# Optimization experiments

Measured on AMD Instinct MI355X. Metric: run time of the kernel, lower is better.

## Reference

```python
import jax, jax.numpy as jnp
import numpy as np

NUM_EXPERTS = 64
Z_LOSS_COEF = 0.001
AUX_LOSS_COEF = 0.001
GROUPS, TOKENS = 64, 8192


def setup_inputs() -> dict:
    key = jax.random.key(0)
    k1, = jax.random.split(key, 1)
    router_logits = jax.random.normal(k1, (GROUPS, TOKENS, NUM_EXPERTS), dtype=jnp.float32)
    attention_mask = jnp.ones((GROUPS, TOKENS), dtype=jnp.int32)  # unused by forward, kept for fidelity
    return {"router_logits": router_logits, "attention_mask": attention_mask, "expert_capacity": 160}


def reference(router_logits, attention_mask, expert_capacity):
    g, t, e = router_logits.shape

    # --- router z-loss: mean over (groups, tokens) of logsumexp^2 ---
    log_z = jax.nn.logsumexp(router_logits, axis=-1)            # [g, t]
    z_loss = jnp.sum(log_z * log_z) / (g * t)

    # --- softmax probs ---
    router_probs = jax.nn.softmax(router_logits, axis=-1)       # [g, t, e]

    # --- recompute expert indices with capacity masking ---
    expert_index = jnp.argmax(router_probs, axis=-1)            # [g, t]
    oh = jax.nn.one_hot(expert_index, e, dtype=jnp.int32)       # [g, t, e]
    token_priority = jnp.cumsum(oh, axis=-2)                    # running count per expert
    capacity_mask = token_priority <= expert_capacity
    oh_masked = oh * capacity_mask.astype(jnp.int32)
    # if token dropped (row all zero), argmax -> 0, matching torch semantics
    expert_index = jnp.argmax(oh_masked, axis=-1)               # [g, t]

    # --- load-balancing aux loss ---
    expert_mask = jax.nn.one_hot(expert_index, e, dtype=jnp.float32)  # [g, t, e]
    tokens_per_group_and_expert = jnp.mean(expert_mask, axis=-2)       # [g, e]
    router_prob_per_group_and_expert = jnp.mean(router_probs, axis=-2) # [g, e]
    aux_loss = jnp.mean(tokens_per_group_and_expert * router_prob_per_group_and_expert) * (e ** 2)

    return Z_LOSS_COEF * z_loss + AUX_LOSS_COEF * aux_loss
```

## Files before the change

kernel.cpp:

```cpp
#include <hip/hip_runtime.h>

#define NG 64
#define NT 8192
#define NE 64
#define Z_COEF 0.001f
#define A_COEF 0.001f

#define BLK 512
#define ITERS 4
#define TPW 64
#define TPB 512
#define NBLK (NG * (NT / TPB))

#define LOG2E 1.44269504088896340736f
#define LN2   0.69314718055994530942f
#define BIGIDX 1048576

#define DPP_XOR1  0xB1
#define DPP_XOR2  0x4E
#define DPP_HMIRR 0x141
#define DPP_MIRR  0x140

template <int CTRL>
__device__ __forceinline__ float fdpp(float x) {
    return __int_as_float(__builtin_amdgcn_mov_dpp(__float_as_int(x), CTRL, 0xF, 0xF, true));
}
template <int CTRL>
__device__ __forceinline__ int idpp(int x) {
    return __builtin_amdgcn_mov_dpp(x, CTRL, 0xF, 0xF, true);
}


__global__ __launch_bounds__(BLK) void router_main(
    const float* __restrict__ logits,
    float* __restrict__ pps,
    unsigned int* __restrict__ pcnt,
    float* __restrict__ pz,
    float* __restrict__ accbuf,
    unsigned int* __restrict__ donep)
{
    const int tid  = threadIdx.x;
    const int lane = tid & 63;
    const int wv   = tid >> 6;
    const int c    = lane & 15;
    const int cb   = c << 2;

    if (blockIdx.x == 0 && tid == 0) {
        accbuf[0] = 0.f;
        accbuf[1] = 0.f;
        *donep    = 0u;
    }

    const int g     = blockIdx.x >> 4;
    const int tbase = (blockIdx.x & 15) * TPB + wv * TPW;

    const float* p0 = logits + ((size_t)g * NT + tbase) * NE + lane * 4;

    __shared__ float        s_ps[NE];
    __shared__ unsigned int s_cnt[NE];
    __shared__ float        s_z;
    if (tid < NE) { s_ps[tid] = 0.f; s_cnt[tid] = 0u; }
    if (tid == 0) s_z = 0.f;
    __syncthreads();

    float accp[4] = {0.f, 0.f, 0.f, 0.f};
    float accz = 0.f;

    for (int it = 0; it < ITERS; ++it) {
        const float* pi = p0 + (size_t)it * 1024;
        float4 cur[4];
#pragma unroll
        for (int k = 0; k < 4; ++k)
            cur[k] = *reinterpret_cast<const float4*>(pi + k * 256);

#pragma unroll
        for (int k = 0; k < 4; ++k) {
            const float v0 = cur[k].x, v1 = cur[k].y, v2 = cur[k].z, v3 = cur[k].w;

            float m = fmaxf(fmaxf(v0, v1), fmaxf(v2, v3));
            m = fmaxf(m, fdpp<DPP_XOR1>(m));
            m = fmaxf(m, fdpp<DPP_XOR2>(m));
            m = fmaxf(m, fdpp<DPP_HMIRR>(m));
            m = fmaxf(m, fdpp<DPP_MIRR>(m));

            const float e0 = exp2f((v0 - m) * LOG2E);
            const float e1 = exp2f((v1 - m) * LOG2E);
            const float e2 = exp2f((v2 - m) * LOG2E);
            const float e3 = exp2f((v3 - m) * LOG2E);
            float s = (e0 + e1) + (e2 + e3);

            int me = BIGIDX;
            if (v3 == m) me = cb + 3;
            if (v2 == m) me = cb + 2;
            if (v1 == m) me = cb + 1;
            if (v0 == m) me = cb + 0;
            me = min(me, idpp<DPP_XOR1>(me));
            me = min(me, idpp<DPP_XOR2>(me));
            me = min(me, idpp<DPP_HMIRR>(me));
            me = min(me, idpp<DPP_MIRR>(me));

            s += fdpp<DPP_XOR1>(s);
            s += fdpp<DPP_XOR2>(s);
            s += fdpp<DPP_HMIRR>(s);
            s += fdpp<DPP_MIRR>(s);

            const float inv = __builtin_amdgcn_rcpf(s);
            accp[0] = fmaf(e0, inv, accp[0]);
            accp[1] = fmaf(e1, inv, accp[1]);
            accp[2] = fmaf(e2, inv, accp[2]);
            accp[3] = fmaf(e3, inv, accp[3]);

            const float lz = fmaf(__log2f(s), LN2, m);
            accz = fmaf(lz, lz, accz);

            if (c == 0)
                atomicAdd(&s_cnt[me], 1u);
        }
    }

#pragma unroll
    for (int j = 0; j < 4; ++j) {
        accp[j] += __shfl_xor(accp[j], 16);
        accp[j] += __shfl_xor(accp[j], 32);
    }
    if (lane < 16) {
#pragma unroll
        for (int j = 0; j < 4; ++j) atomicAdd(&s_ps[cb + j], accp[j]);
    }
    accz += __shfl_xor(accz, 1);
    accz += __shfl_xor(accz, 2);
    accz += __shfl_xor(accz, 4);
    accz += __shfl_xor(accz, 8);
    accz += __shfl_xor(accz, 16);
    accz += __shfl_xor(accz, 32);
    if (lane == 0) atomicAdd(&s_z, accz * 0.0625f);
    __syncthreads();

    const int row = blockIdx.x;
    if (tid < NE) {
        pps [row * NE + tid] = s_ps[tid];
        pcnt[row * NE + tid] = s_cnt[tid];
    }
    if (tid == 0) pz[row] = s_z;
}

__global__ __launch_bounds__(64) void router_final(
    const float* __restrict__ pps,
    const unsigned int* __restrict__ pcnt,
    const float* __restrict__ pz,
    const int* __restrict__ capp,
    float* __restrict__ accbuf,
    unsigned int* __restrict__ donep,
    float* __restrict__ out)
{
    const int lane = threadIdx.x;
    const int g    = blockIdx.x;
    const unsigned int C = (unsigned int)(*capp);

    unsigned int n = 0u;
    float        P = 0.f;
#pragma unroll
    for (int b = 0; b < 16; ++b) {
        const int row = g * 16 + b;
        n += pcnt[row * NE + lane];
        P += pps [row * NE + lane];
    }

    float ovf = (n > C) ? (float)(n - C) : 0.f;
#pragma unroll
    for (int off = 1; off <= 32; off <<= 1) ovf += __shfl_xor(ovf, off);

    float ce = fminf((float)n, (float)C);
    if (lane == 0) ce += ovf;
    float term = ce * P;
#pragma unroll
    for (int off = 1; off <= 32; off <<= 1) term += __shfl_xor(term, off);

    float zz = (lane < 16) ? pz[g * 16 + lane] : 0.f;
#pragma unroll
    for (int off = 1; off <= 8; off <<= 1) zz += __shfl_xor(zz, off);

    if (lane == 0) {
        atomicAdd(&accbuf[0], term);
        atomicAdd(&accbuf[1], zz);
    }
    __threadfence();

    bool last = false;
    if (lane == 0)
        last = (atomicAdd(donep, 1u) == (unsigned int)(NG - 1));

    if (last) {
        const float A = __hip_atomic_load(&accbuf[0], __ATOMIC_RELAXED,
                                          __HIP_MEMORY_SCOPE_AGENT);
        const float Z = __hip_atomic_load(&accbuf[1], __ATOMIC_RELAXED,
                                          __HIP_MEMORY_SCOPE_AGENT);
        const float aux_loss = A * ((float)NE / ((float)NG * (float)NT * (float)NT));
        const float z_loss   = Z / ((float)NG * (float)NT);
        out[0] = Z_COEF * z_loss + A_COEF * aux_loss;
    }
}

extern "C" void kernel_launch(void* const* d_in, const int* in_sizes, int n_in,
                              void* d_out, int out_size, void* d_ws, size_t ws_size,
                              hipStream_t stream)
{
    const float* logits = (const float*)d_in[0];
    const int* cap = (const int*)d_in[2];

    float*        pps    = (float*)d_ws;
    unsigned int* pcnt   = (unsigned int*)((char*)d_ws + (size_t)NBLK * NE * 4);
    float*        pz     = (float*)((char*)d_ws + 2ull * NBLK * NE * 4);
    float*        accbuf = (float*)((char*)d_ws + 2ull * NBLK * NE * 4 + NBLK * 4);
    unsigned int* donep  = (unsigned int*)((char*)d_ws + 2ull * NBLK * NE * 4 + NBLK * 4 + 8);

    router_main<<<NBLK, BLK, 0, stream>>>(logits, pps, pcnt, pz, accbuf, donep);
    router_final<<<NG, 64, 0, stream>>>(pps, pcnt, pz, cap, accbuf, donep,
                                        (float*)d_out);
}
```

Before: 35.18 us.

## Fuse final reduction into main kernel via last-block-per-group counters

Merges the two-kernel pipeline into one launch. Each block publishes its partials with agent-scope atomic stores, then bumps a per-group counter. The last block of each group does the group reduction and bumps a global counter, and the final block writes the loss. This removes the second kernel launch and its dependency gap. In exchange it adds a hipMemsetAsync to reset the counters and relies on relaxed atomics plus a manual waitcnt for ordering.

```diff
diff --git a/kernel.cpp b/kernel.cpp
--- a/kernel.cpp
+++ b/kernel.cpp
@@ -30,14 +30,22 @@
     return __builtin_amdgcn_mov_dpp(x, CTRL, 0xF, 0xF, true);
 }
 
-
-__global__ __launch_bounds__(BLK) void router_main(
+#define ATOMIC_ST_F(p, v) __hip_atomic_store((p), (v), __ATOMIC_RELAXED, __HIP_MEMORY_SCOPE_AGENT)
+#define ATOMIC_ST_U(p, v) __hip_atomic_store((p), (v), __ATOMIC_RELAXED, __HIP_MEMORY_SCOPE_AGENT)
+#define ATOMIC_LD_F(p)    __hip_atomic_load((p), __ATOMIC_RELAXED, __HIP_MEMORY_SCOPE_AGENT)
+#define ATOMIC_LD_U(p)    __hip_atomic_load((p), __ATOMIC_RELAXED, __HIP_MEMORY_SCOPE_AGENT)
+
+
+__global__ __launch_bounds__(BLK) void router_fused(
     const float* __restrict__ logits,
+    const int* __restrict__ capp,
     float* __restrict__ pps,
     unsigned int* __restrict__ pcnt,
     float* __restrict__ pz,
+    unsigned int* __restrict__ gdone,
+    unsigned int* __restrict__ done2,
     float* __restrict__ accbuf,
-    unsigned int* __restrict__ donep)
+    float* __restrict__ out)
 {
     const int tid  = threadIdx.x;
     const int lane = tid & 63;
@@ -45,12 +53,6 @@
     const int c    = lane & 15;
     const int cb   = c << 2;
 
-    if (blockIdx.x == 0 && tid == 0) {
-        accbuf[0] = 0.f;
-        accbuf[1] = 0.f;
-        *donep    = 0u;
-    }
-
     const int g     = blockIdx.x >> 4;
     const int tbase = (blockIdx.x & 15) * TPB + wv * TPW;
 
@@ -59,6 +61,7 @@
     __shared__ float        s_ps[NE];
     __shared__ unsigned int s_cnt[NE];
     __shared__ float        s_z;
+    __shared__ int          s_last;
     if (tid < NE) { s_ps[tid] = 0.f; s_cnt[tid] = 0u; }
     if (tid == 0) s_z = 0.f;
     __syncthreads();
@@ -138,32 +141,30 @@
 
     const int row = blockIdx.x;
     if (tid < NE) {
-        pps [row * NE + tid] = s_ps[tid];
-        pcnt[row * NE + tid] = s_cnt[tid];
-    }
-    if (tid == 0) pz[row] = s_z;
-}
-
-__global__ __launch_bounds__(64) void router_final(
-    const float* __restrict__ pps,
-    const unsigned int* __restrict__ pcnt,
-    const float* __restrict__ pz,
-    const int* __restrict__ capp,
-    float* __restrict__ accbuf,
-    unsigned int* __restrict__ donep,
-    float* __restrict__ out)
-{
-    const int lane = threadIdx.x;
-    const int g    = blockIdx.x;
+        ATOMIC_ST_F(&pps [row * NE + tid], s_ps[tid]);
+        ATOMIC_ST_U(&pcnt[row * NE + tid], s_cnt[tid]);
+    }
+    if (tid == 0) {
+        ATOMIC_ST_F(&pz[row], s_z);
+        asm volatile("s_waitcnt vmcnt(0) lgkmcnt(0)" ::: "memory");
+        const unsigned int old =
+            __hip_atomic_fetch_add(&gdone[g], 1u, __ATOMIC_RELAXED,
+                                   __HIP_MEMORY_SCOPE_AGENT);
+        s_last = (old == 15u);
+    }
+    __syncthreads();
+    if (!s_last) return;
+    if (tid >= 64) return;
+
     const unsigned int C = (unsigned int)(*capp);
 
     unsigned int n = 0u;
     float        P = 0.f;
 #pragma unroll
     for (int b = 0; b < 16; ++b) {
-        const int row = g * 16 + b;
-        n += pcnt[row * NE + lane];
-        P += pps [row * NE + lane];
+        const int r = g * 16 + b;
+        n += ATOMIC_LD_U(&pcnt[r * NE + lane]);
+        P += ATOMIC_LD_F(&pps [r * NE + lane]);
     }
 
     float ovf = (n > C) ? (float)(n - C) : 0.f;
@@ -176,28 +177,27 @@
 #pragma unroll
     for (int off = 1; off <= 32; off <<= 1) term += __shfl_xor(term, off);
 
-    float zz = (lane < 16) ? pz[g * 16 + lane] : 0.f;
+    float zz = (lane < 16) ? ATOMIC_LD_F(&pz[g * 16 + lane]) : 0.f;
 #pragma unroll
     for (int off = 1; off <= 8; off <<= 1) zz += __shfl_xor(zz, off);
 
     if (lane == 0) {
-        atomicAdd(&accbuf[0], term);
-        atomicAdd(&accbuf[1], zz);
-    }
-    __threadfence();
-
-    bool last = false;
-    if (lane == 0)
-        last = (atomicAdd(donep, 1u) == (unsigned int)(NG - 1));
-
-    if (last) {
-        const float A = __hip_atomic_load(&accbuf[0], __ATOMIC_RELAXED,
-                                          __HIP_MEMORY_SCOPE_AGENT);
-        const float Z = __hip_atomic_load(&accbuf[1], __ATOMIC_RELAXED,
-                                          __HIP_MEMORY_SCOPE_AGENT);
-        const float aux_loss = A * ((float)NE / ((float)NG * (float)NT * (float)NT));
-        const float z_loss   = Z / ((float)NG * (float)NT);
-        out[0] = Z_COEF * z_loss + A_COEF * aux_loss;
+        __hip_atomic_fetch_add(&accbuf[0], term, __ATOMIC_RELAXED,
+                               __HIP_MEMORY_SCOPE_AGENT);
+        __hip_atomic_fetch_add(&accbuf[1], zz, __ATOMIC_RELAXED,
+                               __HIP_MEMORY_SCOPE_AGENT);
+        asm volatile("s_waitcnt vmcnt(0) lgkmcnt(0)" ::: "memory");
+        const unsigned int o2 =
+            __hip_atomic_fetch_add(done2, 1u, __ATOMIC_RELAXED,
+                                   __HIP_MEMORY_SCOPE_AGENT);
+        if (o2 == (unsigned int)(NG - 1)) {
+            const float A = ATOMIC_LD_F(&accbuf[0]);
+            const float Z = ATOMIC_LD_F(&accbuf[1]);
+            const float aux_loss =
+                A * ((float)NE / ((float)NG * (float)NT * (float)NT));
+            const float z_loss = Z / ((float)NG * (float)NT);
+            out[0] = Z_COEF * z_loss + A_COEF * aux_loss;
+        }
     }
 }
 
@@ -208,13 +208,17 @@
     const float* logits = (const float*)d_in[0];
     const int* cap = (const int*)d_in[2];
 
-    float*        pps    = (float*)d_ws;
-    unsigned int* pcnt   = (unsigned int*)((char*)d_ws + (size_t)NBLK * NE * 4);
-    float*        pz     = (float*)((char*)d_ws + 2ull * NBLK * NE * 4);
-    float*        accbuf = (float*)((char*)d_ws + 2ull * NBLK * NE * 4 + NBLK * 4);
-    unsigned int* donep  = (unsigned int*)((char*)d_ws + 2ull * NBLK * NE * 4 + NBLK * 4 + 8);
-
-    router_main<<<NBLK, BLK, 0, stream>>>(logits, pps, pcnt, pz, accbuf, donep);
-    router_final<<<NG, 64, 0, stream>>>(pps, pcnt, pz, cap, accbuf, donep,
-                                        (float*)d_out);
-}
+    char* base = (char*)d_ws;
+    float*        pps    = (float*)base;
+    unsigned int* pcnt   = (unsigned int*)(base + (size_t)NBLK * NE * 4);
+    float*        pz     = (float*)(base + 2ull * NBLK * NE * 4);
+    char*         ctr    = base + 2ull * NBLK * NE * 4 + (size_t)NBLK * 4;
+    unsigned int* gdone  = (unsigned int*)ctr;
+    unsigned int* done2  = (unsigned int*)(ctr + NG * 4);
+    float*        accbuf = (float*)(ctr + NG * 4 + 8);
+
+    hipMemsetAsync(ctr, 0, NG * 4 + 8 + 8, stream);
+
+    router_fused<<<NBLK, BLK, 0, stream>>>(logits, cap, pps, pcnt, pz,
+                                           gdone, done2, accbuf, (float*)d_out);
+}
```

After: 40.34 us. +14.7%, slower.

## Stream logits through per-wave LDS ring with async global_load_lds prefetch

Applied to the files above, without the earlier changes.

Replaces the register-staged loads, four float4 per iteration, with a four-slot per-wave LDS ring filled by global_load_lds DMA. Each step waits on vmcnt, reads its slot from LDS, computes, then issues the load for the chunk four steps ahead, so memory traffic overlaps compute across all 16 chunks. This adds 32 KB of LDS per block, which can limit occupancy, plus an extra LDS read per chunk, and it relies on manual waitcnt and sched_barrier ordering being correct.

```diff
diff --git a/kernel.cpp b/kernel.cpp
--- a/kernel.cpp
+++ b/kernel.cpp
@@ -7,7 +7,7 @@
 #define A_COEF 0.001f
 
 #define BLK 512
-#define ITERS 4
+#define NCHUNK 16
 #define TPW 64
 #define TPB 512
 #define NBLK (NG * (NT / TPB))
@@ -29,6 +29,15 @@
 __device__ __forceinline__ int idpp(int x) {
     return __builtin_amdgcn_mov_dpp(x, CTRL, 0xF, 0xF, true);
 }
+
+#define GLL16(gp, lp)                                                        \
+    __builtin_amdgcn_global_load_lds(                                        \
+        (const __attribute__((address_space(1))) void*)(gp),                 \
+        (__attribute__((address_space(3))) void*)(lp), 16, 0, 0)
+
+#define WAITVM(vm)                                                           \
+    asm volatile("s_waitcnt vmcnt(" #vm ")" ::: "memory");                   \
+    __builtin_amdgcn_sched_barrier(0)
 
 
 __global__ __launch_bounds__(BLK) void router_main(
@@ -59,6 +68,8 @@
     __shared__ float        s_ps[NE];
     __shared__ unsigned int s_cnt[NE];
     __shared__ float        s_z;
+    __shared__ __align__(16) unsigned char stage[8][4][1024];
+
     if (tid < NE) { s_ps[tid] = 0.f; s_cnt[tid] = 0u; }
     if (tid == 0) s_z = 0.f;
     __syncthreads();
@@ -66,57 +77,66 @@
     float accp[4] = {0.f, 0.f, 0.f, 0.f};
     float accz = 0.f;
 
-    for (int it = 0; it < ITERS; ++it) {
-        const float* pi = p0 + (size_t)it * 1024;
-        float4 cur[4];
-#pragma unroll
-        for (int k = 0; k < 4; ++k)
-            cur[k] = *reinterpret_cast<const float4*>(pi + k * 256);
-
-#pragma unroll
-        for (int k = 0; k < 4; ++k) {
-            const float v0 = cur[k].x, v1 = cur[k].y, v2 = cur[k].z, v3 = cur[k].w;
-
-            float m = fmaxf(fmaxf(v0, v1), fmaxf(v2, v3));
-            m = fmaxf(m, fdpp<DPP_XOR1>(m));
-            m = fmaxf(m, fdpp<DPP_XOR2>(m));
-            m = fmaxf(m, fdpp<DPP_HMIRR>(m));
-            m = fmaxf(m, fdpp<DPP_MIRR>(m));
-
-            const float e0 = exp2f((v0 - m) * LOG2E);
-            const float e1 = exp2f((v1 - m) * LOG2E);
-            const float e2 = exp2f((v2 - m) * LOG2E);
-            const float e3 = exp2f((v3 - m) * LOG2E);
-            float s = (e0 + e1) + (e2 + e3);
-
-            int me = BIGIDX;
-            if (v3 == m) me = cb + 3;
-            if (v2 == m) me = cb + 2;
-            if (v1 == m) me = cb + 1;
-            if (v0 == m) me = cb + 0;
-            me = min(me, idpp<DPP_XOR1>(me));
-            me = min(me, idpp<DPP_XOR2>(me));
-            me = min(me, idpp<DPP_HMIRR>(me));
-            me = min(me, idpp<DPP_MIRR>(me));
-
-            s += fdpp<DPP_XOR1>(s);
-            s += fdpp<DPP_XOR2>(s);
-            s += fdpp<DPP_HMIRR>(s);
-            s += fdpp<DPP_MIRR>(s);
-
-            const float inv = __builtin_amdgcn_rcpf(s);
-            accp[0] = fmaf(e0, inv, accp[0]);
-            accp[1] = fmaf(e1, inv, accp[1]);
-            accp[2] = fmaf(e2, inv, accp[2]);
-            accp[3] = fmaf(e3, inv, accp[3]);
-
-            const float lz = fmaf(__log2f(s), LN2, m);
-            accz = fmaf(lz, lz, accz);
-
-            if (c == 0)
-                atomicAdd(&s_cnt[me], 1u);
-        }
-    }
+    unsigned char* ring = &stage[wv][0][0];
+
+#pragma unroll
+    for (int b = 0; b < 4; ++b)
+        GLL16(p0 + b * 256, ring + b * 1024);
+
+#define PROC(cv)                                                              \
+    {                                                                         \
+        const float v0 = (cv).x, v1 = (cv).y, v2 = (cv).z, v3 = (cv).w;       \
+        float m = fmaxf(fmaxf(v0, v1), fmaxf(v2, v3));                        \
+        m = fmaxf(m, fdpp<DPP_XOR1>(m));                                      \
+        m = fmaxf(m, fdpp<DPP_XOR2>(m));                                      \
+        m = fmaxf(m, fdpp<DPP_HMIRR>(m));                                     \
+        m = fmaxf(m, fdpp<DPP_MIRR>(m));                                      \
+        const float e0 = exp2f((v0 - m) * LOG2E);                             \
+        const float e1 = exp2f((v1 - m) * LOG2E);                             \
+        const float e2 = exp2f((v2 - m) * LOG2E);                             \
+        const float e3 = exp2f((v3 - m) * LOG2E);                             \
+        float s = (e0 + e1) + (e2 + e3);                                      \
+        int me = BIGIDX;                                                      \
+        if (v3 == m) me = cb + 3;                                             \
+        if (v2 == m) me = cb + 2;                                             \
+        if (v1 == m) me = cb + 1;                                             \
+        if (v0 == m) me = cb + 0;                                             \
+        me = min(me, idpp<DPP_XOR1>(me));                                     \
+        me = min(me, idpp<DPP_XOR2>(me));                                     \
+        me = min(me, idpp<DPP_HMIRR>(me));                                    \
+        me = min(me, idpp<DPP_MIRR>(me));                                     \
+        s += fdpp<DPP_XOR1>(s);                                               \
+        s += fdpp<DPP_XOR2>(s);                                               \
+        s += fdpp<DPP_HMIRR>(s);                                              \
+        s += fdpp<DPP_MIRR>(s);                                               \
+        const float inv = __builtin_amdgcn_rcpf(s);                           \
+        accp[0] = fmaf(e0, inv, accp[0]);                                     \
+        accp[1] = fmaf(e1, inv, accp[1]);                                     \
+        accp[2] = fmaf(e2, inv, accp[2]);                                     \
+        accp[3] = fmaf(e3, inv, accp[3]);                                     \
+        const float lz = fmaf(__log2f(s), LN2, m);                            \
+        accz = fmaf(lz, lz, accz);                                            \
+        if (c == 0) atomicAdd(&s_cnt[me], 1u);                                \
+    }
+
+#define STEP(s, vm)                                                           \
+    {                                                                         \
+        WAITVM(vm);                                                           \
+        const float4 cv = *reinterpret_cast<const float4*>(                   \
+            ring + ((s) & 3) * 1024 + lane * 16);                             \
+        PROC(cv);                                                             \
+        __builtin_amdgcn_sched_barrier(0);                                    \
+        if ((s) + 4 < NCHUNK)                                                 \
+            GLL16(p0 + ((s) + 4) * 256, ring + ((s) & 3) * 1024);             \
+    }
+
+    STEP(0, 3)  STEP(1, 3)  STEP(2, 3)  STEP(3, 3)
+    STEP(4, 3)  STEP(5, 3)  STEP(6, 3)  STEP(7, 3)
+    STEP(8, 3)  STEP(9, 3)  STEP(10, 3) STEP(11, 3)
+    STEP(12, 3) STEP(13, 2) STEP(14, 1) STEP(15, 0)
+
+#undef STEP
+#undef PROC
 
 #pragma unroll
     for (int j = 0; j < 4; ++j) {
```

New measurement: 37.22 us. +5.8%, slower.
